# Kernel optimization log

Hardware: AMD Instinct MI355X
Metric: run time of the kernel (lower is better)

The kernel has to match this reference:

```python
import jax, jax.numpy as jnp
import numpy as np

NUM_EMBEDDINGS = 1024
EMBEDDING_DIM = 256
COMMITMENT_COST = 0.25
DECAY = 0.99
EPS = 1e-05
BATCH = 65536


def setup_inputs() -> dict:
    key = jax.random.key(0)
    k1, k2 = jax.random.split(key, 2)
    z_e = jax.random.normal(k1, (BATCH, EMBEDDING_DIM), dtype=jnp.float32)
    embedding = jax.random.normal(k2, (NUM_EMBEDDINGS, EMBEDDING_DIM), dtype=jnp.float32)
    ema_cluster_size = jnp.zeros((NUM_EMBEDDINGS,), dtype=jnp.float32)
    ema_w = embedding  # buffer initialized as a clone of the codebook
    return {"z_e": z_e, "embedding": embedding,
            "ema_cluster_size": ema_cluster_size, "ema_w": ema_w}


def reference(z_e, embedding, ema_cluster_size, ema_w):
    B, D = z_e.shape
    K = embedding.shape[0]

    # Squared L2 distances: ||z||^2 + ||e||^2 - 2 z.e  -> [B, K]
    z_sq = jnp.sum(z_e * z_e, axis=1, keepdims=True)          # [B, 1]
    e_sq = jnp.sum(embedding * embedding, axis=1)[None, :]    # [1, K]
    ze = jnp.matmul(z_e, embedding.T)                         # [B, K]
    distances = z_sq + e_sq - 2.0 * ze

    encoding_indices = jnp.argmin(distances, axis=1)          # [B]

    # Gather instead of one-hot matmul (same math as encodings @ embedding)
    z_q = embedding[encoding_indices]                         # [B, D]
    z_q_st = z_e + jax.lax.stop_gradient(z_q - z_e)

    vq_loss = COMMITMENT_COST * jnp.mean(
        (jax.lax.stop_gradient(z_q) - z_e) ** 2)

    # EMA statistics (training-mode update); segment_sum == one-hot reductions
    cluster_size = jax.ops.segment_sum(
        jnp.ones((B,), dtype=z_e.dtype), encoding_indices, num_segments=K)
    new_ema_cluster_size = DECAY * ema_cluster_size + (1.0 - DECAY) * cluster_size
    dw = jax.ops.segment_sum(z_e, encoding_indices, num_segments=K)  # [K, D]
    new_ema_w = DECAY * ema_w + (1.0 - DECAY) * dw

    n = jnp.sum(new_ema_cluster_size)
    smoothed = (new_ema_cluster_size + EPS) / (n + K * EPS) * n
    new_embedding = new_ema_w / smoothed[:, None]

    avg_probs = cluster_size / B
    perplexity = jnp.exp(-jnp.sum(avg_probs * jnp.log(avg_probs + 1e-10)))

    return (z_q_st, vq_loss, perplexity, encoding_indices,
            new_embedding, new_ema_cluster_size, new_ema_w)
```

## Files before the change

### kernel.cpp

```cpp
#include <hip/hip_runtime.h>
#include <hip/hip_bf16.h>
#include <math.h>

#define BATCH 65536
#define DIM 256
#define KC 1024
#define COMMIT 0.25f
#define DECAY 0.99f
#define EPSV 1e-5f

#define O_ZQ   0
#define O_LOSS 16777216
#define O_PERP 16777217
#define O_IDX  16777218
#define O_EMB  16842754
#define O_NCS  17104898
#define O_NEW  17105922

typedef __attribute__((ext_vector_type(8))) short bf16x8;
typedef __attribute__((ext_vector_type(4))) float f32x4;

typedef __attribute__((address_space(1))) const void* as1_cvp;
typedef __attribute__((address_space(3))) void* as3_vp;

__device__ __forceinline__ void gload_lds16(const void* g, void* l) {
    __builtin_amdgcn_global_load_lds((as1_cvp)g, (as3_vp)l, 16, 0, 0);
}

__device__ __forceinline__ unsigned short bf16_rne(float x) {
    unsigned u = __builtin_bit_cast(unsigned, x);
    unsigned r = (u + 0x7FFFu + ((u >> 16) & 1u)) >> 16;
    return (unsigned short)r;
}
__device__ __forceinline__ float bf16_to_f(unsigned short h) {
    unsigned u = ((unsigned)h) << 16;
    return __builtin_bit_cast(float, u);
}

__global__ __launch_bounds__(256) void prep_zero_kernel(
        const float* __restrict__ emb,
        unsigned short* __restrict__ ehi, unsigned short* __restrict__ elo,
        float* __restrict__ e_sq, float* __restrict__ dw,
        int* __restrict__ counts, float* __restrict__ out) {
    int k = blockIdx.x;
    int t = threadIdx.x;
    dw[(size_t)k * DIM + t] = 0.0f;
    if (t == 64) counts[k] = 0;
    if (k == 0 && t == 128) out[O_LOSS] = 0.0f;
    if (t < 64) {
        int lane = t;
        const float4* ep = (const float4*)(emb + (size_t)k * DIM);
        float4 e = ep[lane];
        float x[4] = {e.x, e.y, e.z, e.w};
        unsigned h[4], l[4];
        float s = 0.0f;
        #pragma unroll
        for (int j = 0; j < 4; ++j) {
            h[j] = bf16_rne(x[j]);
            l[j] = bf16_rne(x[j] - bf16_to_f((unsigned short)h[j]));
            s += x[j] * x[j];
        }
        uint2 ph = make_uint2(h[0] | (h[1] << 16), h[2] | (h[3] << 16));
        uint2 pl = make_uint2(l[0] | (l[1] << 16), l[2] | (l[3] << 16));
        int slot = lane >> 1;
        int half = lane & 1;
        int us = k * 256 + ((slot ^ (k & 7)) << 3) + (half << 2);
        *(uint2*)(ehi + us) = ph;
        *(uint2*)(elo + us) = pl;
        for (int off = 32; off; off >>= 1) s += __shfl_down(s, off, 64);
        if (lane == 0) e_sq[k] = s;
    }
}

#define CH_ROWS 16
__global__ __launch_bounds__(256, 2) void argmin_kernel(
        const float* __restrict__ z_e,
        const unsigned short* __restrict__ ehi,
        const unsigned short* __restrict__ elo,
        const float* __restrict__ e_sq,
        int* __restrict__ idx_out, float* __restrict__ idx_f_out,
        int* __restrict__ counts) {
    __shared__ __align__(16) unsigned short bhi_s[2][CH_ROWS * 256];
    __shared__ __align__(16) unsigned short blo_s[2][CH_ROWS * 256];
    __shared__ float esq_s[KC];

    int tid = threadIdx.x;
    int w = tid >> 6;
    int lane = tid & 63;
    int m16 = lane & 15;
    int quad = lane >> 4;
    int base_m = blockIdx.x * 128 + w * 32;

#define STAGE(c, b) { \
    const char* gh_ = (const char*)ehi + (c) * 8192 + tid * 16; \
    const char* gl_ = (const char*)elo + (c) * 8192 + tid * 16; \
    char* lh_ = (char*)(bhi_s[b]) + tid * 16; \
    char* ll_ = (char*)(blo_s[b]) + tid * 16; \
    _Pragma("unroll") for (int r_ = 0; r_ < 2; ++r_) { \
        gload_lds16(gh_ + r_ * 4096, lh_ + r_ * 4096); \
        gload_lds16(gl_ + r_ * 4096, ll_ + r_ * 4096); } }

    STAGE(0, 0)

    #pragma unroll
    for (int i = 0; i < 4; ++i) esq_s[tid + i * 256] = e_sq[tid + i * 256];

    bf16x8 ahi[2][8], alo[2][8];
    #pragma unroll
    for (int f = 0; f < 2; ++f) {
        const float* zr = z_e + (size_t)(base_m + f * 16 + m16) * DIM;
        #pragma unroll
        for (int ks = 0; ks < 8; ++ks) {
            const float4* p = (const float4*)(zr + ks * 32 + quad * 8);
            float4 x0 = p[0], x1 = p[1];
            float xs[8] = {x0.x, x0.y, x0.z, x0.w, x1.x, x1.y, x1.z, x1.w};
            #pragma unroll
            for (int j = 0; j < 8; ++j) {
                unsigned short h = bf16_rne(xs[j]);
                unsigned short l = bf16_rne(xs[j] - bf16_to_f(h));
                ahi[f][ks][j] = (short)h;
                alo[f][ks][j] = (short)l;
            }
        }
    }

    float best0[4] = {1e30f, 1e30f, 1e30f, 1e30f};
    float best1[4] = {1e30f, 1e30f, 1e30f, 1e30f};
    int bk0[4] = {0, 0, 0, 0};
    int bk1[4] = {0, 0, 0, 0};

    const int rsw = (m16 & 7) << 3;

#define COMPUTE(c, b) { \
    f32x4 acc0 = {0.f, 0.f, 0.f, 0.f}; \
    f32x4 acc1 = {0.f, 0.f, 0.f, 0.f}; \
    const unsigned short* bh_row = bhi_s[b] + m16 * 256; \
    const unsigned short* bl_row = blo_s[b] + m16 * 256; \
    _Pragma("unroll") for (int ks_ = 0; ks_ < 8; ++ks_) { \
        int us_off = (((ks_ * 4 + quad) << 3) ^ rsw); \
        bf16x8 bh = *(const bf16x8*)(bh_row + us_off); \
        bf16x8 bl = *(const bf16x8*)(bl_row + us_off); \
        acc0 = __builtin_amdgcn_mfma_f32_16x16x32_bf16(ahi[0][ks_], bh, acc0, 0, 0, 0); \
        acc1 = __builtin_amdgcn_mfma_f32_16x16x32_bf16(ahi[1][ks_], bh, acc1, 0, 0, 0); \
        acc0 = __builtin_amdgcn_mfma_f32_16x16x32_bf16(ahi[0][ks_], bl, acc0, 0, 0, 0); \
        acc1 = __builtin_amdgcn_mfma_f32_16x16x32_bf16(ahi[1][ks_], bl, acc1, 0, 0, 0); \
        acc0 = __builtin_amdgcn_mfma_f32_16x16x32_bf16(alo[0][ks_], bh, acc0, 0, 0, 0); \
        acc1 = __builtin_amdgcn_mfma_f32_16x16x32_bf16(alo[1][ks_], bh, acc1, 0, 0, 0); } \
    int col = (c) * 16 + m16; \
    float es = esq_s[col]; \
    _Pragma("unroll") for (int r_ = 0; r_ < 4; ++r_) { \
        float d0 = es - 2.0f * acc0[r_]; \
        float d1 = es - 2.0f * acc1[r_]; \
        if (d0 < best0[r_]) { best0[r_] = d0; bk0[r_] = col; } \
        if (d1 < best1[r_]) { best1[r_] = d1; bk1[r_] = col; } } }

    __syncthreads();

    for (int c = 0; c < 64; c += 2) {
        STAGE(c + 1, 1)
        COMPUTE(c, 0)
        __syncthreads();
        if (c + 2 < 64) STAGE(c + 2, 0)
        COMPUTE(c + 1, 1)
        __syncthreads();
    }

    #pragma unroll
    for (int off = 1; off < 16; off <<= 1) {
        #pragma unroll
        for (int r = 0; r < 4; ++r) {
            float ov0 = __shfl_xor(best0[r], off, 64);
            int   ok0 = __shfl_xor(bk0[r], off, 64);
            if (ov0 < best0[r] || (ov0 == best0[r] && ok0 < bk0[r])) { best0[r] = ov0; bk0[r] = ok0; }
            float ov1 = __shfl_xor(best1[r], off, 64);
            int   ok1 = __shfl_xor(bk1[r], off, 64);
            if (ov1 < best1[r] || (ov1 == best1[r] && ok1 < bk1[r])) { best1[r] = ov1; bk1[r] = ok1; }
        }
    }
    if (m16 == 0) {
        #pragma unroll
        for (int r = 0; r < 4; ++r) {
            int row0 = base_m + quad * 4 + r;
            int row1 = base_m + 16 + quad * 4 + r;
            idx_out[row0] = bk0[r];
            idx_f_out[row0] = (float)bk0[r];
            idx_out[row1] = bk1[r];
            idx_f_out[row1] = (float)bk1[r];
            atomicAdd(&counts[bk0[r]], 1);
            atomicAdd(&counts[bk1[r]], 1);
        }
    }
#undef STAGE
#undef COMPUTE
}

__global__ __launch_bounds__(1024) void prefix_stats_kernel(
        const int* __restrict__ counts, int* __restrict__ cursor,
        const float* __restrict__ ema_cs, float* __restrict__ out,
        float* __restrict__ n_ws) {
    __shared__ int wsum[16];
    __shared__ float s1[1024];
    __shared__ float s2[1024];
    int t = threadIdx.x;
    int lane = t & 63;
    int wv = t >> 6;
    int c = counts[t];
    int x = c;
    #pragma unroll
    for (int off = 1; off < 64; off <<= 1) {
        int v = __shfl_up(x, off, 64);
        if (lane >= off) x += v;
    }
    if (lane == 63) wsum[wv] = x;
    float cf = (float)c;
    float ncs = DECAY * ema_cs[t] + (1.0f - DECAY) * cf;
    out[O_NCS + t] = ncs;
    float p = cf / (float)BATCH;
    s1[t] = ncs;
    s2[t] = p * logf(p + 1e-10f);
    __syncthreads();
    if (wv == 0) {
        int v = (lane < 16) ? wsum[lane] : 0;
        #pragma unroll
        for (int off = 1; off < 16; off <<= 1) {
            int u = __shfl_up(v, off, 64);
            if (lane >= off) v += u;
        }
        if (lane < 16) wsum[lane] = v;
    }
    __syncthreads();
    int woff = (wv == 0) ? 0 : wsum[wv - 1];
    cursor[t] = woff + x - c;
    for (int s = 512; s; s >>= 1) {
        if (t < s) { s1[t] += s1[t + s]; s2[t] += s2[t + s]; }
        __syncthreads();
    }
    if (t == 0) {
        n_ws[0] = s1[0];
        out[O_PERP] = expf(-s2[0]);
    }
}

__global__ __launch_bounds__(256) void scatter_rows_kernel(
        const int* __restrict__ idx, int* __restrict__ cursor,
        int* __restrict__ sorted_rows) {
    int i = blockIdx.x * 256 + threadIdx.x;
    int k = idx[i];
    int pos = atomicAdd(&cursor[k], 1);
    sorted_rows[pos] = i;
}

#define SEG 64
__global__ __launch_bounds__(256) void dw_zq_kernel(
        const float* __restrict__ z_e, const float* __restrict__ emb,
        const int* __restrict__ idx, const int* __restrict__ sorted_rows,
        float* __restrict__ zq_out, float* __restrict__ dw,
        float* __restrict__ out) {
    __shared__ int rows_s[SEG];
    __shared__ int keys_s[SEG];
    int t = threadIdx.x;
    int w = t >> 6;
    int lane = t & 63;
    int base = blockIdx.x * SEG;
    if (t < SEG) {
        int r = sorted_rows[base + t];
        rows_s[t] = r;
        keys_s[t] = idx[r];
    }
    __syncthreads();

    int c4 = lane * 4;
    float4 acc = make_float4(0.f, 0.f, 0.f, 0.f);
    float lsum = 0.0f;
    int kprev = keys_s[w * 16];
    #pragma unroll
    for (int g = 0; g < 2; ++g) {
        int rowb[8], kb[8];
        float4 zb[8], qb[8];
        #pragma unroll
        for (int u = 0; u < 8; ++u) {
            int i = w * 16 + g * 8 + u;
            rowb[u] = rows_s[i];
            kb[u] = keys_s[i];
        }
        #pragma unroll
        for (int u = 0; u < 8; ++u) {
            zb[u] = *(const float4*)(z_e + (size_t)rowb[u] * DIM + c4);
            qb[u] = *(const float4*)(emb + (size_t)kb[u] * DIM + c4);
        }
        #pragma unroll
        for (int u = 0; u < 8; ++u) {
            float4 z = zb[u], q = qb[u];
            float4 d = make_float4(q.x - z.x, q.y - z.y, q.z - z.z, q.w - z.w);
            float4 o = make_float4(z.x + d.x, z.y + d.y, z.z + d.z, z.w + d.w);
            *(float4*)(zq_out + (size_t)rowb[u] * DIM + c4) = o;
            lsum += d.x * d.x + d.y * d.y + d.z * d.z + d.w * d.w;
            if (kb[u] != kprev) {
                float* dst = dw + (size_t)kprev * DIM + c4;
                atomicAdd(dst + 0, acc.x);
                atomicAdd(dst + 1, acc.y);
                atomicAdd(dst + 2, acc.z);
                atomicAdd(dst + 3, acc.w);
                acc = make_float4(0.f, 0.f, 0.f, 0.f);
                kprev = kb[u];
            }
            acc.x += z.x; acc.y += z.y; acc.z += z.z; acc.w += z.w;
        }
    }
    {
        float* dst = dw + (size_t)kprev * DIM + c4;
        atomicAdd(dst + 0, acc.x);
        atomicAdd(dst + 1, acc.y);
        atomicAdd(dst + 2, acc.z);
        atomicAdd(dst + 3, acc.w);
    }

    __shared__ float red[256];
    red[t] = lsum;
    __syncthreads();
    for (int s = 128; s; s >>= 1) {
        if (t < s) red[t] += red[t + s];
        __syncthreads();
    }
    if (t == 0)
        atomicAdd(out + O_LOSS, red[0] * (COMMIT / ((float)BATCH * (float)DIM)));
}

__global__ __launch_bounds__(256) void finalize_emb(
        const float* __restrict__ ema_w, const float* __restrict__ dw,
        const float* __restrict__ ncs_arr, const float* __restrict__ n_ws,
        float* __restrict__ out_emb, float* __restrict__ out_emaw) {
    int k = blockIdx.x;
    int d = threadIdx.x;
    size_t i = (size_t)k * DIM + d;
    float w = DECAY * ema_w[i] + (1.0f - DECAY) * dw[i];
    out_emaw[i] = w;
    float n = n_ws[0];
    float ncs = ncs_arr[k];
    float smoothed = (ncs + EPSV) / (n + (float)KC * EPSV) * n;
    out_emb[i] = w / smoothed;
}

extern "C" void kernel_launch(void* const* d_in, const int* in_sizes, int n_in,
                              void* d_out, int out_size, void* d_ws, size_t ws_size,
                              hipStream_t stream) {
    const float* z_e    = (const float*)d_in[0];
    const float* emb    = (const float*)d_in[1];
    const float* ema_cs = (const float*)d_in[2];
    const float* ema_w  = (const float*)d_in[3];
    float* out = (float*)d_out;
    float* ws = (float*)d_ws;

    float* dw            = ws;
    unsigned short* ehi  = (unsigned short*)(dw + KC * DIM);
    unsigned short* elo  = ehi + KC * DIM;
    float* e_sq          = (float*)(elo + KC * DIM);
    int* idx             = (int*)(e_sq + KC);
    int* counts          = idx + BATCH;
    int* cursor          = counts + KC;
    int* sorted_rows     = cursor + KC;
    float* n_ws          = (float*)(sorted_rows + BATCH);

    prep_zero_kernel<<<dim3(KC), dim3(256), 0, stream>>>(
        emb, ehi, elo, e_sq, dw, counts, out);
    argmin_kernel<<<dim3(BATCH / 128), dim3(256), 0, stream>>>(
        z_e, ehi, elo, e_sq, idx, out + O_IDX, counts);
    prefix_stats_kernel<<<dim3(1), dim3(1024), 0, stream>>>(
        counts, cursor, ema_cs, out, n_ws);
    scatter_rows_kernel<<<dim3(BATCH / 256), dim3(256), 0, stream>>>(
        idx, cursor, sorted_rows);
    dw_zq_kernel<<<dim3(BATCH / SEG), dim3(256), 0, stream>>>(
        z_e, emb, idx, sorted_rows, out + O_ZQ, dw, out);
    finalize_emb<<<dim3(KC), dim3(256), 0, stream>>>(
        ema_w, dw, out + O_NCS, n_ws, out + O_EMB, out + O_NEW);
}
```

Baseline: 325.7 us.

## Split argmin over codebook halves and combine partial minima in a new kernel

The argmin kernel now launches twice as many blocks, each scanning half of the codebook for its 128 rows. Each block writes a packed 64-bit key per row (order-preserving float distance in the high bits, index in the low bits). A new combine kernel takes the smaller of the two keys per row, writes the indices, and builds counts with a shared-memory histogram before issuing global atomics. This raises grid-level parallelism and cuts global atomic traffic. The cost is that the z_e fragment load and bf16 split are done twice per row, plus an extra launch and a 1 MB partial buffer.

```diff
diff --git a/kernel.cpp b/kernel.cpp
--- a/kernel.cpp
+++ b/kernel.cpp
@@ -35,6 +35,10 @@
 __device__ __forceinline__ float bf16_to_f(unsigned short h) {
     unsigned u = ((unsigned)h) << 16;
     return __builtin_bit_cast(float, u);
+}
+__device__ __forceinline__ unsigned enc_f32(float f) {
+    unsigned u = __builtin_bit_cast(unsigned, f);
+    return u ^ ((unsigned)((int)u >> 31) | 0x80000000u);
 }
 
 __global__ __launch_bounds__(256) void prep_zero_kernel(
@@ -78,22 +82,24 @@
         const unsigned short* __restrict__ ehi,
         const unsigned short* __restrict__ elo,
         const float* __restrict__ e_sq,
-        int* __restrict__ idx_out, float* __restrict__ idx_f_out,
-        int* __restrict__ counts) {
+        unsigned long long* __restrict__ part) {
     __shared__ __align__(16) unsigned short bhi_s[2][CH_ROWS * 256];
     __shared__ __align__(16) unsigned short blo_s[2][CH_ROWS * 256];
-    __shared__ float esq_s[KC];
+    __shared__ float esq_s[512];
 
     int tid = threadIdx.x;
     int w = tid >> 6;
     int lane = tid & 63;
     int m16 = lane & 15;
     int quad = lane >> 4;
-    int base_m = blockIdx.x * 128 + w * 32;
+    int half = blockIdx.x & 1;
+    int base_m = (blockIdx.x >> 1) * 128 + w * 32;
+    const char* ehi_b = (const char*)ehi + half * 262144;
+    const char* elo_b = (const char*)elo + half * 262144;
 
 #define STAGE(c, b) { \
-    const char* gh_ = (const char*)ehi + (c) * 8192 + tid * 16; \
-    const char* gl_ = (const char*)elo + (c) * 8192 + tid * 16; \
+    const char* gh_ = ehi_b + (c) * 8192 + tid * 16; \
+    const char* gl_ = elo_b + (c) * 8192 + tid * 16; \
     char* lh_ = (char*)(bhi_s[b]) + tid * 16; \
     char* ll_ = (char*)(blo_s[b]) + tid * 16; \
     _Pragma("unroll") for (int r_ = 0; r_ < 2; ++r_) { \
@@ -102,8 +108,8 @@
 
     STAGE(0, 0)
 
-    #pragma unroll
-    for (int i = 0; i < 4; ++i) esq_s[tid + i * 256] = e_sq[tid + i * 256];
+    esq_s[tid] = e_sq[(half << 9) + tid];
+    esq_s[tid + 256] = e_sq[(half << 9) + tid + 256];
 
     bf16x8 ahi[2][8], alo[2][8];
     #pragma unroll
@@ -146,8 +152,9 @@
         acc1 = __builtin_amdgcn_mfma_f32_16x16x32_bf16(ahi[1][ks_], bl, acc1, 0, 0, 0); \
         acc0 = __builtin_amdgcn_mfma_f32_16x16x32_bf16(alo[0][ks_], bh, acc0, 0, 0, 0); \
         acc1 = __builtin_amdgcn_mfma_f32_16x16x32_bf16(alo[1][ks_], bh, acc1, 0, 0, 0); } \
-    int col = (c) * 16 + m16; \
-    float es = esq_s[col]; \
+    int lcol = (c) * 16 + m16; \
+    int col = (half << 9) + lcol; \
+    float es = esq_s[lcol]; \
     _Pragma("unroll") for (int r_ = 0; r_ < 4; ++r_) { \
         float d0 = es - 2.0f * acc0[r_]; \
         float d1 = es - 2.0f * acc1[r_]; \
@@ -156,11 +163,11 @@
 
     __syncthreads();
 
-    for (int c = 0; c < 64; c += 2) {
+    for (int c = 0; c < 32; c += 2) {
         STAGE(c + 1, 1)
         COMPUTE(c, 0)
         __syncthreads();
-        if (c + 2 < 64) STAGE(c + 2, 0)
+        if (c + 2 < 32) STAGE(c + 2, 0)
         COMPUTE(c + 1, 1)
         __syncthreads();
     }
@@ -182,16 +189,42 @@
         for (int r = 0; r < 4; ++r) {
             int row0 = base_m + quad * 4 + r;
             int row1 = base_m + 16 + quad * 4 + r;
-            idx_out[row0] = bk0[r];
-            idx_f_out[row0] = (float)bk0[r];
-            idx_out[row1] = bk1[r];
-            idx_f_out[row1] = (float)bk1[r];
-            atomicAdd(&counts[bk0[r]], 1);
-            atomicAdd(&counts[bk1[r]], 1);
+            unsigned long long k0 =
+                ((unsigned long long)enc_f32(best0[r]) << 32) | (unsigned)bk0[r];
+            unsigned long long k1 =
+                ((unsigned long long)enc_f32(best1[r]) << 32) | (unsigned)bk1[r];
+            part[row0 * 2 + half] = k0;
+            part[row1 * 2 + half] = k1;
         }
     }
 #undef STAGE
 #undef COMPUTE
+}
+
+__global__ __launch_bounds__(256) void combine_kernel(
+        const unsigned long long* __restrict__ part,
+        int* __restrict__ idx_out, float* __restrict__ idx_f_out,
+        int* __restrict__ counts) {
+    __shared__ int h[KC];
+    int t = threadIdx.x;
+    #pragma unroll
+    for (int i = t; i < KC; i += 256) h[i] = 0;
+    __syncthreads();
+    int base = blockIdx.x * 512;
+    #pragma unroll
+    for (int j = 0; j < 2; ++j) {
+        int row = base + j * 256 + t;
+        unsigned long long k0 = part[row * 2];
+        unsigned long long k1 = part[row * 2 + 1];
+        unsigned long long m = k0 < k1 ? k0 : k1;
+        int k = (int)(m & 0xFFFFFFFFu);
+        idx_out[row] = k;
+        idx_f_out[row] = (float)k;
+        atomicAdd(&h[k], 1);
+    }
+    __syncthreads();
+    #pragma unroll
+    for (int i = t; i < KC; i += 256) if (h[i]) atomicAdd(&counts[i], h[i]);
 }
 
 __global__ __launch_bounds__(1024) void prefix_stats_kernel(
@@ -354,7 +387,8 @@
     float* dw            = ws;
     unsigned short* ehi  = (unsigned short*)(dw + KC * DIM);
     unsigned short* elo  = ehi + KC * DIM;
-    float* e_sq          = (float*)(elo + KC * DIM);
+    unsigned long long* part = (unsigned long long*)(elo + KC * DIM);
+    float* e_sq          = (float*)(part + 2 * BATCH);
     int* idx             = (int*)(e_sq + KC);
     int* counts          = idx + BATCH;
     int* cursor          = counts + KC;
@@ -363,8 +397,10 @@
 
     prep_zero_kernel<<<dim3(KC), dim3(256), 0, stream>>>(
         emb, ehi, elo, e_sq, dw, counts, out);
-    argmin_kernel<<<dim3(BATCH / 128), dim3(256), 0, stream>>>(
-        z_e, ehi, elo, e_sq, idx, out + O_IDX, counts);
+    argmin_kernel<<<dim3(BATCH / 128 * 2), dim3(256), 0, stream>>>(
+        z_e, ehi, elo, e_sq, part);
+    combine_kernel<<<dim3(BATCH / 512), dim3(256), 0, stream>>>(
+        part, idx, out + O_IDX, counts);
     prefix_stats_kernel<<<dim3(1), dim3(1024), 0, stream>>>(
         counts, cursor, ema_cs, out, n_ws);
     scatter_rows_kernel<<<dim3(BATCH / 256), dim3(256), 0, stream>>>(
```

Result: faster. 308.3 us (-5.3%).
